# Optimization experiments

Measured on AMD Instinct MI355X. Metric: run time of the kernel, lower is better.

## Reference

```python
import jax, jax.numpy as jnp
import numpy as np

VOCAB, E, H, L, B, OUT = 50000, 300, 300, 75, 2048, 5

def setup_inputs() -> dict:
    key = jax.random.key(0)
    ks = jax.random.split(key, 12)
    s_e = 1.0 / np.sqrt(E)
    s_h = 1.0 / np.sqrt(H)
    return {
        "input_sequences": jax.random.randint(ks[0], (B, L), 0, VOCAB),
        "emb": jax.random.normal(ks[1], (VOCAB, E), jnp.float32) * 0.1,
        "W_ih": jax.random.normal(ks[2], (3 * H, E), jnp.float32) * s_e,
        "W_hh": jax.random.normal(ks[3], (3 * H, H), jnp.float32) * s_h,
        "b_ih": jax.random.normal(ks[4], (3 * H,), jnp.float32) * s_h,
        "b_hh": jax.random.normal(ks[5], (3 * H,), jnp.float32) * s_h,
        "wCo_w": jax.random.normal(ks[6], (3 * H,), jnp.float32) * (1.0 / np.sqrt(3 * H)),
        "wCo_b": jax.random.normal(ks[7], (1,), jnp.float32) * 0.02,
        "Wmy_w": jax.random.normal(ks[8], (L,), jnp.float32) * (1.0 / np.sqrt(L)),
        "Wmy_b": jax.random.normal(ks[9], (1,), jnp.float32) * 0.02,
        "logits_w": jax.random.normal(ks[10], (OUT, H), jnp.float32) * s_h,
        "logits_b": jax.random.normal(ks[11], (OUT,), jnp.float32) * 0.02,
    }

def _gru(x_tm, W_ih, W_hh, b_ih, b_hh):
    # x_tm: (L, B, E) time-major. PyTorch GRU cell math.
    gx_all = jnp.einsum("lbe,ge->lbg", x_tm, W_ih) + b_ih  # (L, B, 3H)
    h0 = jnp.zeros((x_tm.shape[1], W_hh.shape[1]), x_tm.dtype)
    def step(h, gx):
        gh = h @ W_hh.T + b_hh
        xr, xz, xn = jnp.split(gx, 3, axis=-1)
        hr, hz, hn = jnp.split(gh, 3, axis=-1)
        r = jax.nn.sigmoid(xr + hr)
        z = jax.nn.sigmoid(xz + hz)
        n = jnp.tanh(xn + r * hn)
        h_new = (1.0 - z) * n + z * h
        return h_new, h_new
    _, ys = jax.lax.scan(step, h0, gx_all)
    return ys  # (L, B, H)

def reference(input_sequences, emb, W_ih, W_hh, b_ih, b_hh,
              wCo_w, wCo_b, Wmy_w, Wmy_b, logits_w, logits_b):
    x = emb[input_sequences]                      # (B, L, E)
    out_tm = _gru(x.transpose(1, 0, 2), W_ih, W_hh, b_ih, b_hh)  # (L, B, H)
    h = out_tm.transpose(1, 0, 2)                 # (B, L, H)
    # co_attention: s_ij = wCo @ cat(h_i, h_j, h_i*h_j) + b
    # computed WITHOUT materializing the (B, L, L, 3H) tensor:
    wa, wb, wc = jnp.split(wCo_w, 3)
    a = h @ wa                                    # (B, L)
    b = h @ wb                                    # (B, L)
    c = jnp.einsum("bid,bjd->bij", h * wc, h)     # (B, L, L)
    s = a[:, :, None] + b[:, None, :] + c + wCo_b[0]
    # zero the diagonal (mask = ones - diag)
    s = s * (1.0 - jnp.eye(s.shape[1], dtype=s.dtype))
    # Wmy: Linear(75, 1) over the j axis
    sm = s @ Wmy_w + Wmy_b[0]                     # (B, L)
    attn = jax.nn.softmax(sm, axis=1)             # softmax over i
    pooled = jnp.einsum("bi,bih->bh", attn, h)    # (B, H)
    return pooled @ logits_w.T + logits_b         # (B, OUT)
```

## Files before the change

### kernel.cpp

```cpp
#include <hip/hip_runtime.h>
#include <stdint.h>


typedef float f32x4 __attribute__((ext_vector_type(4)));
typedef short bf16x8 __attribute__((ext_vector_type(8)));
typedef unsigned short u16;
typedef u16 u16x8 __attribute__((ext_vector_type(8)));
typedef u16 u16x4 __attribute__((ext_vector_type(4)));

#define DI __device__ __forceinline__

DI float bf2f(u16 v) {
    uint32_t u = ((uint32_t)v) << 16;
    float f;
    __builtin_memcpy(&f, &u, 4);
    return f;
}
DI u16 f2bf(float f) {
    uint32_t u;
    __builtin_memcpy(&u, &f, 4);
    uint32_t r = u + 0x7fffu + ((u >> 16) & 1u);
    return (u16)(r >> 16);
}
DI u16 cvt1(const void* p, int i, int f32m) {
    return f32m ? f2bf(((const float*)p)[i]) : ((const u16*)p)[i];
}

DI int hswz(int L, int kt) { return L ^ kt ^ (((L >> 4) & 3) << 1); }

DI u16x8 load_row8(const u16* __restrict__ base, int e0) {
    u16x4 z = {0, 0, 0, 0};
    u16x4 lo = (e0 < 300) ? *(const u16x4*)(base + e0) : z;
    u16x4 hi = (e0 + 4 < 300) ? *(const u16x4*)(base + e0 + 4) : z;
    u16x8 r;
    r[0] = lo[0]; r[1] = lo[1]; r[2] = lo[2]; r[3] = lo[3];
    r[4] = hi[0]; r[5] = hi[1]; r[6] = hi[2]; r[7] = hi[3];
    return r;
}
DI u16x8 load_row8_f32(const float* __restrict__ base, int e0) {
    f32x4 z = {0.f, 0.f, 0.f, 0.f};
    f32x4 lo = (e0 < 300) ? *(const f32x4*)(base + e0) : z;
    f32x4 hi = (e0 + 4 < 300) ? *(const f32x4*)(base + e0 + 4) : z;
    u16x8 r;
    r[0] = f2bf(lo[0]); r[1] = f2bf(lo[1]); r[2] = f2bf(lo[2]); r[3] = f2bf(lo[3]);
    r[4] = f2bf(hi[0]); r[5] = f2bf(hi[1]); r[6] = f2bf(hi[2]); r[7] = f2bf(hi[3]);
    return r;
}

__global__ __launch_bounds__(256) void detect_dtype(const u16* __restrict__ raw,
                                                    int* __restrict__ flag) {
    __shared__ int cnt;
    if (threadIdx.x == 0) cnt = 0;
    __syncthreads();
    int local = 0;
    for (int i = threadIdx.x; i < 4096; i += 256) {
        int e = (raw[i] >> 7) & 0xFF;
        if (e >= 140) local++;
    }
    atomicAdd(&cnt, local);
    __syncthreads();
    if (threadIdx.x == 0) flag[0] = (cnt > 256) ? 1 : 0;
}

__global__ __launch_bounds__(256) void conv_big(const void* __restrict__ in,
                                                u16* __restrict__ outp, int n,
                                                const int* __restrict__ flag) {
    const int f32m = flag[0];
    int i0 = (blockIdx.x * 256 + threadIdx.x) * 8;
#pragma unroll
    for (int k = 0; k < 8; k++) {
        int i = i0 + k;
        if (i < n) outp[i] = cvt1(in, i, f32m);
    }
}

__global__ __launch_bounds__(256) void conv_smalls(
    const void* bih_r, const void* bhh_r, const void* wCo_r, const void* wCob_r,
    const void* Wmy_r, const void* Wmyb_r, const void* lw_r, const void* lb_r,
    u16* __restrict__ smalls, const int* __restrict__ flag) {
    const int f32m = flag[0];
    int t = blockIdx.x * 256 + threadIdx.x;
    if (t < 900) smalls[t] = cvt1(bih_r, t, f32m);
    else if (t < 1800) smalls[1024 + t - 900] = cvt1(bhh_r, t - 900, f32m);
    else if (t < 2700) smalls[2048 + t - 1800] = cvt1(wCo_r, t - 1800, f32m);
    else if (t < 2775) smalls[3072 + t - 2700] = cvt1(Wmy_r, t - 2700, f32m);
    else if (t < 4275) smalls[3200 + t - 2775] = cvt1(lw_r, t - 2775, f32m);
    else if (t < 4280) smalls[4704 + t - 4275] = cvt1(lb_r, t - 4275, f32m);
    else if (t == 4280) smalls[4712] = cvt1(wCob_r, 0, f32m);
    else if (t == 4281) smalls[4713] = cvt1(Wmyb_r, 0, f32m);
}

__global__ __launch_bounds__(256) void prep_img(const u16* __restrict__ W,
                                                u16* __restrict__ img) {
    int t = blockIdx.x * 256 + threadIdx.x;
    if (t >= 60 * 10 * 64) return;
    int lane = t & 63;
    int kt = (t >> 6) % 10;
    int nt = t / 640;
    int g = nt * 16 + (lane & 15);
    int gate = g / 320, u = g - gate * 320;
    int e0 = kt * 32 + (lane >> 4) * 8;
    u16x8 v;
    if (u < 300) {
        v = load_row8(W + (size_t)(gate * 300 + u) * 300, e0);
    } else {
        u16x8 z = {0, 0, 0, 0, 0, 0, 0, 0};
        v = z;
    }
    *(u16x8*)&img[(size_t)t * 8] = v;
}

__global__ __launch_bounds__(256) void zero_hstate(float* __restrict__ hs) {
    int t = blockIdx.x * 256 + threadIdx.x;
    f32x4 z = {0.f, 0.f, 0.f, 0.f};
    ((f32x4*)hs)[t] = z;
}

__global__ __launch_bounds__(256, 2) void gemm1_kernel(
    const int* __restrict__ seq, const void* __restrict__ emb_raw,
    const u16* __restrict__ Wimg, const u16* __restrict__ bih,
    _Float16* __restrict__ gxn, int ck, int phase, int BC, int bshift,
    const int* __restrict__ flag) {
    __shared__ int ids[192];
    __shared__ __align__(16) u16 Aimg[12 * 64 * 8];
    __shared__ __align__(16) u16 Bbuf[12 * 64 * 8];

    const int tid = threadIdx.x;
    const int lane = tid & 63, wv = tid >> 6, q = lane >> 4, c = lane & 15;
    const int m0 = blockIdx.x * 192;
    const int nb = blockIdx.y;
    const int f32m = flag[0];
    const size_t PL = (size_t)15 * BC * 320;

    if (tid < 192) {
        int m = m0 + tid;
        int bc = m & (BC - 1);
        int tp = m >> bshift;
        ids[tid] = seq[(size_t)(phase * BC + bc) * 75 + ck * 15 + tp];
    }
    __syncthreads();

    f32x4 acc[3][12];
#pragma unroll
    for (int mt = 0; mt < 3; mt++)
#pragma unroll
        for (int nt = 0; nt < 12; nt++) {
            f32x4 z = {0.f, 0.f, 0.f, 0.f};
            acc[mt][nt] = z;
        }

    for (int kt = 0; kt < 10; kt++) {
#pragma unroll
        for (int s = 0; s < 3; s++) {
            int o = tid + s * 256;
            int qq = o / 192;
            int r = o - qq * 192;
            int e0 = kt * 32 + qq * 8;
            u16x8 v = f32m ? load_row8_f32((const float*)emb_raw + (size_t)ids[r] * 300, e0)
                           : load_row8((const u16*)emb_raw + (size_t)ids[r] * 300, e0);
            *(u16x8*)&Aimg[(((r >> 4) * 64) + ((r & 15) | (qq << 4))) * 8] = v;
        }
#pragma unroll
        for (int s = 0; s < 3; s++) {
            int ch = tid + s * 256;
            *(u16x8*)&Bbuf[ch * 8] =
                *(const u16x8*)&Wimg[(((size_t)(nb * 12 + (ch >> 6)) * 10 + kt) * 64 + (ch & 63)) * 8];
        }
        __syncthreads();

        bf16x8 a[3];
#pragma unroll
        for (int mt = 0; mt < 3; mt++) {
            u16x8 tmp = *(const u16x8*)&Aimg[(((wv * 3 + mt) * 64) + lane) * 8];
            a[mt] = __builtin_bit_cast(bf16x8, tmp);
        }
#pragma unroll
        for (int nt = 0; nt < 12; nt++) {
            u16x8 tb = *(const u16x8*)&Bbuf[(nt * 64 + lane) * 8];
            bf16x8 b = __builtin_bit_cast(bf16x8, tb);
#pragma unroll
            for (int mt = 0; mt < 3; mt++)
                acc[mt][nt] = __builtin_amdgcn_mfma_f32_16x16x32_bf16(a[mt], b, acc[mt][nt], 0, 0, 0);
        }
        __syncthreads();
    }

#pragma unroll
    for (int nt = 0; nt < 12; nt++) {
        int g = nb * 192 + nt * 16 + c;
        int gate = g / 320, u = g - gate * 320;
        float bias = (u < 300) ? bf2f(bih[gate * 300 + u]) : 0.f;
        _Float16* gp = gxn + (size_t)gate * PL;
#pragma unroll
        for (int mt = 0; mt < 3; mt++) {
            int mrow = m0 + (wv * 3 + mt) * 16 + q * 4;
#pragma unroll
            for (int reg = 0; reg < 4; reg++) {
                gp[(size_t)(mrow + reg) * 320 + u] = (_Float16)(acc[mt][nt][reg] + bias);
            }
        }
    }
}

__global__ __launch_bounds__(640, 1) void gru_chunk(
    const _Float16* __restrict__ gxn, const u16* __restrict__ Wimg,
    const u16* __restrict__ bhh_g, u16* __restrict__ h_all,
    float* __restrict__ hstate, int ck, int BC) {
    __shared__ __align__(16) u16 Hhi[10 * 64 * 8];
    __shared__ __align__(16) u16 Hlo[10 * 64 * 8];
    __shared__ __align__(16) u16 Wlds[61440];

    const int tid = threadIdx.x;
    const int lane = tid & 63, wv = tid >> 6, q = lane >> 4, c = lane & 15;
    const int b0 = blockIdx.x * 16;
    const int wbase = wv * 6144;
    const size_t PL = (size_t)15 * BC * 320;

    auto STAGE = [&](int kt, int buf) {
        u16* dst = &Wlds[wbase + buf * 3072];
#pragma unroll
        for (int Ti = 0; Ti < 2; Ti++)
#pragma unroll
            for (int g = 0; g < 3; g++) {
                int nt = g * 20 + (wv + 10 * Ti);
                __builtin_amdgcn_global_load_lds(
                    (const unsigned int*)(Wimg + (size_t)(nt * 10 + kt) * 512 + lane * 8),
                    (unsigned int*)(dst + (Ti * 3 + g) * 512), 16, 0, 0);
            }
    };

    STAGE(0, 0);

    float bhh[2][3];
    float hm[2][4];
#pragma unroll
    for (int Ti = 0; Ti < 2; Ti++) {
        int T = wv + 10 * Ti;
        int u = T * 16 + c;
#pragma unroll
        for (int g = 0; g < 3; g++)
            bhh[Ti][g] = (u < 300) ? bf2f(bhh_g[g * 300 + u]) : 0.f;
        int kti = T >> 1;
        int qp = ((T & 1) << 1) | (c >> 3);
        int j = c & 7;
#pragma unroll
        for (int reg = 0; reg < 4; reg++) {
            int m = q * 4 + reg;
            float h = hstate[(size_t)(b0 + m) * 320 + u];
            hm[Ti][reg] = h;
            int idx = (kti * 64 + ((q * 4 + reg) | (qp << 4))) * 8 + j;
            u16 hi = f2bf(h);
            Hhi[idx] = hi;
            Hlo[idx] = f2bf(h - bf2f(hi));
        }
    }
    __syncthreads();

    for (int tt = 0; tt < 15; tt++) {
        STAGE(1, 1);

        float gxr[2][4], gxz[2][4], gxnv[2][4];
#pragma unroll
        for (int Ti = 0; Ti < 2; Ti++) {
            int u = (wv + 10 * Ti) * 16 + c;
#pragma unroll
            for (int reg = 0; reg < 4; reg++) {
                int m = q * 4 + reg;
                size_t idx = (size_t)((size_t)tt * BC + b0 + m) * 320 + u;
                gxr[Ti][reg] = (float)gxn[idx];
                gxz[Ti][reg] = (float)gxn[PL + idx];
                gxnv[Ti][reg] = (float)gxn[2 * PL + idx];
            }
        }

        f32x4 acc[2][3];
#pragma unroll
        for (int Ti = 0; Ti < 2; Ti++)
#pragma unroll
            for (int g = 0; g < 3; g++) {
                f32x4 z = {0.f, 0.f, 0.f, 0.f};
                acc[Ti][g] = z;
            }

#pragma unroll 2
        for (int kt = 0; kt < 10; kt++) {
            if (kt >= 1 && kt < 9) STAGE(kt + 1, (kt + 1) & 1);
            else if (kt == 9 && tt < 14) STAGE(0, 0);

            if (kt == 9 && tt == 14) {
                asm volatile("s_waitcnt vmcnt(0)" ::: "memory");
            } else if (kt < 2) {
                asm volatile("s_waitcnt vmcnt(30)" ::: "memory");
            } else {
                asm volatile("s_waitcnt vmcnt(6)" ::: "memory");
            }

            u16x8 th = *(const u16x8*)&Hhi[(kt * 64 + lane) * 8];
            u16x8 tl = *(const u16x8*)&Hlo[(kt * 64 + lane) * 8];
            bf16x8 ahi = __builtin_bit_cast(bf16x8, th);
            bf16x8 alo = __builtin_bit_cast(bf16x8, tl);
            const u16* wb = &Wlds[wbase + (kt & 1) * 3072];
#pragma unroll
            for (int Ti = 0; Ti < 2; Ti++)
#pragma unroll
                for (int g = 0; g < 3; g++) {
                    u16x8 tb = *(const u16x8*)&wb[(Ti * 3 + g) * 512 + lane * 8];
                    bf16x8 b = __builtin_bit_cast(bf16x8, tb);
                    acc[Ti][g] = __builtin_amdgcn_mfma_f32_16x16x32_bf16(
                        ahi, b, acc[Ti][g], 0, 0, 0);
                    acc[Ti][g] = __builtin_amdgcn_mfma_f32_16x16x32_bf16(
                        alo, b, acc[Ti][g], 0, 0, 0);
                }
        }

        const int tglob = ck * 15 + tt;
#pragma unroll
        for (int Ti = 0; Ti < 2; Ti++) {
            int u = (wv + 10 * Ti) * 16 + c;
#pragma unroll
            for (int reg = 0; reg < 4; reg++) {
                int m = q * 4 + reg;
                float xr = gxr[Ti][reg];
                float xz = gxz[Ti][reg];
                float xn = gxnv[Ti][reg];
                float hr = acc[Ti][0][reg] + bhh[Ti][0];
                float hz = acc[Ti][1][reg] + bhh[Ti][1];
                float hn = acc[Ti][2][reg] + bhh[Ti][2];
                float r = 1.f / (1.f + __expf(-(xr + hr)));
                float z = 1.f / (1.f + __expf(-(xz + hz)));
                float ex = __expf(2.f * (xn + r * hn));
                float n = 1.f - 2.f / (ex + 1.f);
                float h = (1.f - z) * n + z * hm[Ti][reg];
                hm[Ti][reg] = h;
                h_all[((size_t)tglob * BC + (b0 + m)) * 320 + u] = f2bf(h);
            }
        }
        __syncthreads();

#pragma unroll
        for (int Ti = 0; Ti < 2; Ti++) {
            int T = wv + 10 * Ti;
            int kti = T >> 1;
            int qp = ((T & 1) << 1) | (c >> 3);
            int j = c & 7;
#pragma unroll
            for (int reg = 0; reg < 4; reg++) {
                int idx = (kti * 64 + ((q * 4 + reg) | (qp << 4))) * 8 + j;
                float h = hm[Ti][reg];
                u16 hi = f2bf(h);
                Hhi[idx] = hi;
                Hlo[idx] = f2bf(h - bf2f(hi));
            }
        }
        __syncthreads();
    }

#pragma unroll
    for (int Ti = 0; Ti < 2; Ti++) {
        int u = (wv + 10 * Ti) * 16 + c;
#pragma unroll
        for (int reg = 0; reg < 4; reg++) {
            int m = q * 4 + reg;
            hstate[(size_t)(b0 + m) * 320 + u] = hm[Ti][reg];
        }
    }
}

__global__ __launch_bounds__(256) void coattn_kernel(
    const u16* __restrict__ h_all, const u16* __restrict__ smalls,
    void* __restrict__ outv, const int* __restrict__ flag, int phase, int BC) {
    __shared__ __align__(16) u16 himg[5 * 10 * 64 * 8];
    __shared__ float smacc[80], aArr[80], bArr[80], diagArr[80], attn[80], smv[80];
    __shared__ float scal[2];
    __shared__ float logitsAcc[5];

    const u16* wCo = smalls + 2048;
    const u16* Wmy = smalls + 3072;
    const u16* lw = smalls + 3200;
    const u16* lb = smalls + 4704;
    const int f32out = flag[0];

    const int b = blockIdx.x;
    const int tid = threadIdx.x;
    const int lane = tid & 63, wv = tid >> 6, q = lane >> 4, c = lane & 15;

    for (int o = tid; o < 3200; o += 256) {
        int i = o / 40;
        int oc = o - i * 40;
        int kt = oc >> 2, qq = oc & 3;
        int e0 = kt * 32 + qq * 8;
        u16x8 v = {0, 0, 0, 0, 0, 0, 0, 0};
        if (i < 75) v = *(const u16x8*)(h_all + ((size_t)i * BC + b) * 320 + e0);
        *(u16x8*)&himg[(((i >> 4) * 10 + kt) * 64 + hswz((i & 15) | (qq << 4), kt)) * 8] = v;
    }
    if (tid < 80) {
        smacc[tid] = 0.f; aArr[tid] = 0.f; bArr[tid] = 0.f;
        diagArr[tid] = 0.f; attn[tid] = 0.f;
    }
    if (tid < 5) logitsAcc[tid] = 0.f;
    __syncthreads();

    for (int pass = 0; pass < 2; pass++) {
        int nt = (pass == 0) ? wv : 4;
        int jj = nt * 16 + c;
        bf16x8 bfr[10];
#pragma unroll
        for (int kt = 0; kt < 10; kt++) {
            int e0 = kt * 32 + q * 8;
            u16x8 res = {0, 0, 0, 0, 0, 0, 0, 0};
            if (jj < 75) {
                u16x8 hv = *(const u16x8*)&himg[((nt * 10 + kt) * 64 + hswz(lane, kt)) * 8];
                u16x8 wcv = load_row8(wCo + 600, e0);
#pragma unroll
                for (int j = 0; j < 8; j++) res[j] = f2bf(bf2f(hv[j]) * bf2f(wcv[j]));
            } else if (jj == 75) {
                res = load_row8(wCo, e0);
            } else if (jj == 76) {
                res = load_row8(wCo + 300, e0);
            }
            bfr[kt] = __builtin_bit_cast(bf16x8, res);
        }
        float wmyj = (jj < 75) ? bf2f(Wmy[jj]) : 0.f;

        int nmt = (pass == 0) ? 5 : (wv == 0 ? 2 : 1);
        for (int mi = 0; mi < nmt; mi++) {
            int mt = (pass == 0) ? mi : (wv == 0 ? mi * 4 : wv);
            f32x4 acc = {0.f, 0.f, 0.f, 0.f};
#pragma unroll
            for (int kt = 0; kt < 10; kt++) {
                u16x8 ta = *(const u16x8*)&himg[((mt * 10 + kt) * 64 + hswz(lane, kt)) * 8];
                bf16x8 a = __builtin_bit_cast(bf16x8, ta);
                acc = __builtin_amdgcn_mfma_f32_16x16x32_bf16(a, bfr[kt], acc, 0, 0, 0);
            }
#pragma unroll
            for (int reg = 0; reg < 4; reg++) {
                int i = mt * 16 + q * 4 + reg;
                float v = acc[reg];
                float p = v * wmyj;
                p += __shfl_xor(p, 1);
                p += __shfl_xor(p, 2);
                p += __shfl_xor(p, 4);
                p += __shfl_xor(p, 8);
                if (c == 0 && i < 75) atomicAdd(&smacc[i], p);
                if (jj == i && i < 75) diagArr[i] = v;
                if (jj == 75) aArr[i] = v;
                if (jj == 76) bArr[i] = v;
            }
        }
    }
    __syncthreads();

    if (tid < 64) {
        float w1 = bf2f(Wmy[tid]);
        float w2 = (tid + 64 < 75) ? bf2f(Wmy[tid + 64]) : 0.f;
        float s1 = w1 + w2;
        float s2 = w1 * bArr[tid] + ((tid + 64 < 75) ? w2 * bArr[tid + 64] : 0.f);
#pragma unroll
        for (int m = 1; m < 64; m <<= 1) {
            s1 += __shfl_xor(s1, m);
            s2 += __shfl_xor(s2, m);
        }
        if (tid == 0) { scal[0] = s1; scal[1] = s2; }
    }
    __syncthreads();

    float cb = bf2f(smalls[4712]);
    float wmyb = bf2f(smalls[4713]);
    if (tid < 75) {
        float Wi = bf2f(Wmy[tid]);
        smv[tid] = smacc[tid] - diagArr[tid] * Wi + (aArr[tid] + cb) * (scal[0] - Wi) +
                   scal[1] - bArr[tid] * Wi + wmyb;
    }
    __syncthreads();

    if (tid < 64) {
        float v1 = smv[tid];
        float v2 = (tid + 64 < 75) ? smv[tid + 64] : -1e30f;
        float mx = fmaxf(v1, v2);
#pragma unroll
        for (int m = 1; m < 64; m <<= 1) mx = fmaxf(mx, __shfl_xor(mx, m));
        float e1 = __expf(v1 - mx);
        float e2 = (tid + 64 < 75) ? __expf(v2 - mx) : 0.f;
        float s = e1 + e2;
#pragma unroll
        for (int m = 1; m < 64; m <<= 1) s += __shfl_xor(s, m);
        attn[tid] = e1 / s;
        if (tid + 64 < 75) attn[tid + 64] = e2 / s;
    }
    __syncthreads();

    const int d1 = tid, d2 = tid + 256;
    float pd1 = 0.f, pd2 = 0.f;
    {
        const int kt1 = d1 >> 5, qq1 = (d1 >> 3) & 3, j1 = d1 & 7;
        const int kt2 = d2 >> 5, qq2 = (d2 >> 3) & 3, j2 = d2 & 7;
        for (int i = 0; i < 75; i++) {
            float a = attn[i];
            int ih = i >> 4, il = i & 15;
            pd1 += a * bf2f(himg[((ih * 10 + kt1) * 64 + hswz(il | (qq1 << 4), kt1)) * 8 + j1]);
            if (wv == 0)
                pd2 += a * bf2f(himg[((ih * 10 + kt2) * 64 + hswz(il | (qq2 << 4), kt2)) * 8 + j2]);
        }
    }
#pragma unroll
    for (int o = 0; o < 5; o++) {
        float part = (d1 < 300) ? pd1 * bf2f(lw[o * 300 + d1]) : 0.f;
        if (wv == 0 && d2 < 300) part += pd2 * bf2f(lw[o * 300 + d2]);
#pragma unroll
        for (int m = 1; m < 64; m <<= 1) part += __shfl_xor(part, m);
        if (lane == 0) atomicAdd(&logitsAcc[o], part);
    }
    __syncthreads();

    if (tid < 5) {
        float v = logitsAcc[tid] + bf2f(lb[tid]);
        size_t idx = (size_t)(phase * BC + b) * 5 + tid;
        if (f32out) ((float*)outv)[idx] = v;
        else ((u16*)outv)[idx] = f2bf(v);
    }
}

extern "C" void kernel_launch(void* const* d_in, const int* in_sizes, int n_in,
                              void* d_out, int out_size, void* d_ws, size_t ws_size,
                              hipStream_t stream) {
    const int* seq = (const int*)d_in[0];

    char* p = (char*)d_ws;
    int* flag = (int*)p;
    u16* smalls = (u16*)(p + 16);
    u16* WihImg = (u16*)(p + 9488);
    u16* WhhImg = (u16*)(p + 623888);
    u16* Wih_c = (u16*)(p + 1238288);
    u16* Whh_c = (u16*)(p + 1778288);
    const unsigned long long fixed_end = 2318288ull;

    auto req = [&](long long BC) -> unsigned long long {
        return fixed_end + (unsigned long long)BC * 87680ull + 1048576ull;
    };
    int BC = 256, bshift = 8;
    if (ws_size >= req(2048)) { BC = 2048; bshift = 11; }
    else if (ws_size >= req(1024)) { BC = 1024; bshift = 10; }
    else if (ws_size >= req(512)) { BC = 512; bshift = 9; }
    const int P = 2048 / BC;

    unsigned long long gx_b = 15ull * BC * 2560ull;
    unsigned long long h_b = 75ull * BC * 640ull;
    _Float16* gxn = (_Float16*)(p + fixed_end);
    u16* h_all = (u16*)(p + fixed_end + gx_b);
    float* hstate = (float*)(p + fixed_end + gx_b + h_b);

    detect_dtype<<<dim3(1), dim3(256), 0, stream>>>((const u16*)d_in[1], flag);
    conv_big<<<dim3((270000 + 2047) / 2048), dim3(256), 0, stream>>>(
        d_in[2], Wih_c, 270000, flag);
    conv_big<<<dim3((270000 + 2047) / 2048), dim3(256), 0, stream>>>(
        d_in[3], Whh_c, 270000, flag);
    conv_smalls<<<dim3(17), dim3(256), 0, stream>>>(
        d_in[4], d_in[5], d_in[6], d_in[7], d_in[8], d_in[9], d_in[10], d_in[11],
        smalls, flag);

    prep_img<<<dim3(150), dim3(256), 0, stream>>>(Wih_c, WihImg);
    prep_img<<<dim3(150), dim3(256), 0, stream>>>(Whh_c, WhhImg);

    for (int phase = 0; phase < P; phase++) {
        zero_hstate<<<dim3(BC * 320 / 1024), dim3(256), 0, stream>>>(hstate);
        for (int ck = 0; ck < 5; ck++) {
            gemm1_kernel<<<dim3(15 * BC / 192, 5), dim3(256), 0, stream>>>(
                seq, d_in[1], WihImg, smalls , gxn, ck, phase, BC, bshift, flag);
            gru_chunk<<<dim3(BC / 16), dim3(640), 0, stream>>>(
                gxn, WhhImg, smalls + 1024 , h_all, hstate, ck, BC);
        }
        coattn_kernel<<<dim3(BC), dim3(256), 0, stream>>>(h_all, smalls, d_out, flag,
                                                          phase, BC);
    }
}
```

Measured before the change: 1.275 ms.

## Double-buffer GRU hidden state, split weight staging between LDS and registers, vectorize gx

```diff
diff --git a/kernel.cpp b/kernel.cpp
--- a/kernel.cpp
+++ b/kernel.cpp
@@ -4,6 +4,7 @@
 
 typedef float f32x4 __attribute__((ext_vector_type(4)));
 typedef short bf16x8 __attribute__((ext_vector_type(8)));
+typedef _Float16 f16x4 __attribute__((ext_vector_type(4)));
 typedef unsigned short u16;
 typedef u16 u16x8 __attribute__((ext_vector_type(8)));
 typedef u16 u16x4 __attribute__((ext_vector_type(4)));
@@ -194,10 +195,11 @@
 #pragma unroll
         for (int mt = 0; mt < 3; mt++) {
             int mrow = m0 + (wv * 3 + mt) * 16 + q * 4;
-#pragma unroll
-            for (int reg = 0; reg < 4; reg++) {
-                gp[(size_t)(mrow + reg) * 320 + u] = (_Float16)(acc[mt][nt][reg] + bias);
-            }
+            f16x4 v;
+#pragma unroll
+            for (int reg = 0; reg < 4; reg++)
+                v[reg] = (_Float16)(acc[mt][nt][reg] + bias);
+            *(f16x4*)&gp[((size_t)(mrow >> 2) * 320 + u) * 4] = v;
         }
     }
 }
@@ -206,27 +208,32 @@
     const _Float16* __restrict__ gxn, const u16* __restrict__ Wimg,
     const u16* __restrict__ bhh_g, u16* __restrict__ h_all,
     float* __restrict__ hstate, int ck, int BC) {
-    __shared__ __align__(16) u16 Hhi[10 * 64 * 8];
-    __shared__ __align__(16) u16 Hlo[10 * 64 * 8];
-    __shared__ __align__(16) u16 Wlds[61440];
+    __shared__ __align__(16) u16 Hhi[2][10 * 64 * 8];
+    __shared__ __align__(16) u16 Hlo[2][10 * 64 * 8];
+    __shared__ __align__(16) u16 Wlds[30720];
 
     const int tid = threadIdx.x;
     const int lane = tid & 63, wv = tid >> 6, q = lane >> 4, c = lane & 15;
     const int b0 = blockIdx.x * 16;
-    const int wbase = wv * 6144;
+    const int wbase = wv * 3072;
     const size_t PL = (size_t)15 * BC * 320;
 
+    u16x8 wreg[2][3];
+
     auto STAGE = [&](int kt, int buf) {
-        u16* dst = &Wlds[wbase + buf * 3072];
-#pragma unroll
-        for (int Ti = 0; Ti < 2; Ti++)
-#pragma unroll
-            for (int g = 0; g < 3; g++) {
-                int nt = g * 20 + (wv + 10 * Ti);
-                __builtin_amdgcn_global_load_lds(
-                    (const unsigned int*)(Wimg + (size_t)(nt * 10 + kt) * 512 + lane * 8),
-                    (unsigned int*)(dst + (Ti * 3 + g) * 512), 16, 0, 0);
-            }
+        u16* dst = &Wlds[wbase + buf * 1536];
+#pragma unroll
+        for (int g = 0; g < 3; g++) {
+            int nt0 = g * 20 + wv;
+            __builtin_amdgcn_global_load_lds(
+                (const unsigned int*)(Wimg + (size_t)(nt0 * 10 + kt) * 512 + lane * 8),
+                (unsigned int*)(dst + g * 512), 16, 0, 0);
+        }
+#pragma unroll
+        for (int g = 0; g < 3; g++) {
+            int nt1 = g * 20 + wv + 10;
+            wreg[buf][g] = *(const u16x8*)&Wimg[(size_t)(nt1 * 10 + kt) * 512 + lane * 8];
+        }
     };
 
     STAGE(0, 0);
@@ -250,27 +257,26 @@
             hm[Ti][reg] = h;
             int idx = (kti * 64 + ((q * 4 + reg) | (qp << 4))) * 8 + j;
             u16 hi = f2bf(h);
-            Hhi[idx] = hi;
-            Hlo[idx] = f2bf(h - bf2f(hi));
+            Hhi[0][idx] = hi;
+            Hlo[0][idx] = f2bf(h - bf2f(hi));
         }
     }
     __syncthreads();
 
     for (int tt = 0; tt < 15; tt++) {
+        const int rd = tt & 1, wr = rd ^ 1;
+
         STAGE(1, 1);
 
-        float gxr[2][4], gxz[2][4], gxnv[2][4];
+        f16x4 gv[2][3];
+        const size_t rg = ((size_t)tt * BC + b0) >> 2;
 #pragma unroll
         for (int Ti = 0; Ti < 2; Ti++) {
             int u = (wv + 10 * Ti) * 16 + c;
-#pragma unroll
-            for (int reg = 0; reg < 4; reg++) {
-                int m = q * 4 + reg;
-                size_t idx = (size_t)((size_t)tt * BC + b0 + m) * 320 + u;
-                gxr[Ti][reg] = (float)gxn[idx];
-                gxz[Ti][reg] = (float)gxn[PL + idx];
-                gxnv[Ti][reg] = (float)gxn[2 * PL + idx];
-            }
+            size_t base = ((rg + q) * 320 + u) * 4;
+#pragma unroll
+            for (int g = 0; g < 3; g++)
+                gv[Ti][g] = *(const f16x4*)&gxn[(size_t)g * PL + base];
         }
 
         f32x4 acc[2][3];
@@ -282,7 +288,7 @@
                 acc[Ti][g] = z;
             }
 
-#pragma unroll 2
+#pragma unroll
         for (int kt = 0; kt < 10; kt++) {
             if (kt >= 1 && kt < 9) STAGE(kt + 1, (kt + 1) & 1);
             else if (kt == 9 && tt < 14) STAGE(0, 0);
@@ -290,39 +296,46 @@
             if (kt == 9 && tt == 14) {
                 asm volatile("s_waitcnt vmcnt(0)" ::: "memory");
             } else if (kt < 2) {
-                asm volatile("s_waitcnt vmcnt(30)" ::: "memory");
+                asm volatile("s_waitcnt vmcnt(12)" ::: "memory");
             } else {
                 asm volatile("s_waitcnt vmcnt(6)" ::: "memory");
             }
 
-            u16x8 th = *(const u16x8*)&Hhi[(kt * 64 + lane) * 8];
-            u16x8 tl = *(const u16x8*)&Hlo[(kt * 64 + lane) * 8];
+            u16x8 th = *(const u16x8*)&Hhi[rd][(kt * 64 + lane) * 8];
+            u16x8 tl = *(const u16x8*)&Hlo[rd][(kt * 64 + lane) * 8];
             bf16x8 ahi = __builtin_bit_cast(bf16x8, th);
             bf16x8 alo = __builtin_bit_cast(bf16x8, tl);
-            const u16* wb = &Wlds[wbase + (kt & 1) * 3072];
-#pragma unroll
-            for (int Ti = 0; Ti < 2; Ti++)
-#pragma unroll
-                for (int g = 0; g < 3; g++) {
-                    u16x8 tb = *(const u16x8*)&wb[(Ti * 3 + g) * 512 + lane * 8];
-                    bf16x8 b = __builtin_bit_cast(bf16x8, tb);
-                    acc[Ti][g] = __builtin_amdgcn_mfma_f32_16x16x32_bf16(
-                        ahi, b, acc[Ti][g], 0, 0, 0);
-                    acc[Ti][g] = __builtin_amdgcn_mfma_f32_16x16x32_bf16(
-                        alo, b, acc[Ti][g], 0, 0, 0);
-                }
+            const u16* wb = &Wlds[wbase + (kt & 1) * 1536];
+#pragma unroll
+            for (int g = 0; g < 3; g++) {
+                u16x8 tb = *(const u16x8*)&wb[g * 512 + lane * 8];
+                bf16x8 b0f = __builtin_bit_cast(bf16x8, tb);
+                acc[0][g] = __builtin_amdgcn_mfma_f32_16x16x32_bf16(
+                    ahi, b0f, acc[0][g], 0, 0, 0);
+                acc[0][g] = __builtin_amdgcn_mfma_f32_16x16x32_bf16(
+                    alo, b0f, acc[0][g], 0, 0, 0);
+                bf16x8 b1f = __builtin_bit_cast(bf16x8, wreg[kt & 1][g]);
+                acc[1][g] = __builtin_amdgcn_mfma_f32_16x16x32_bf16(
+                    ahi, b1f, acc[1][g], 0, 0, 0);
+                acc[1][g] = __builtin_amdgcn_mfma_f32_16x16x32_bf16(
+                    alo, b1f, acc[1][g], 0, 0, 0);
+            }
         }
 
         const int tglob = ck * 15 + tt;
 #pragma unroll
         for (int Ti = 0; Ti < 2; Ti++) {
-            int u = (wv + 10 * Ti) * 16 + c;
+            int T = wv + 10 * Ti;
+            int u = T * 16 + c;
+            int kti = T >> 1;
+            int qp = ((T & 1) << 1) | (c >> 3);
+            int j = c & 7;
 #pragma unroll
             for (int reg = 0; reg < 4; reg++) {
                 int m = q * 4 + reg;
-                float xr = gxr[Ti][reg];
-                float xz = gxz[Ti][reg];
-                float xn = gxnv[Ti][reg];
+                float xr = (float)gv[Ti][0][reg];
+                float xz = (float)gv[Ti][1][reg];
+                float xn = (float)gv[Ti][2][reg];
                 float hr = acc[Ti][0][reg] + bhh[Ti][0];
                 float hz = acc[Ti][1][reg] + bhh[Ti][1];
                 float hn = acc[Ti][2][reg] + bhh[Ti][2];
@@ -333,23 +346,10 @@
                 float h = (1.f - z) * n + z * hm[Ti][reg];
                 hm[Ti][reg] = h;
                 h_all[((size_t)tglob * BC + (b0 + m)) * 320 + u] = f2bf(h);
-            }
-        }
-        __syncthreads();
-
-#pragma unroll
-        for (int Ti = 0; Ti < 2; Ti++) {
-            int T = wv + 10 * Ti;
-            int kti = T >> 1;
-            int qp = ((T & 1) << 1) | (c >> 3);
-            int j = c & 7;
-#pragma unroll
-            for (int reg = 0; reg < 4; reg++) {
                 int idx = (kti * 64 + ((q * 4 + reg) | (qp << 4))) * 8 + j;
-                float h = hm[Ti][reg];
                 u16 hi = f2bf(h);
-                Hhi[idx] = hi;
-                Hlo[idx] = f2bf(h - bf2f(hi));
+                Hhi[wr][idx] = hi;
+                Hlo[wr][idx] = f2bf(h - bf2f(hi));
             }
         }
         __syncthreads();
```

After: 1.853 ms. 45.3% more time.
